# Performance work log

Measured on AMD Instinct MI355X. Metric: run time of the kernel, lower is better.

The kernel has to match this reference:

```python
import jax, jax.numpy as jnp
import numpy as np

NUM_HEADS = 16

def setup_inputs() -> dict:
    key = jax.random.key(0)
    k1, k2, k3 = jax.random.split(key, 3)
    B, N, C = 4, 1024, 1024
    x = jax.random.normal(k1, (B, N, C), dtype=jnp.float32)
    w_qkv = jax.random.normal(k2, (C, 3 * C), dtype=jnp.float32) * (C ** -0.5)
    b_qkv = jnp.zeros((3 * C,), dtype=jnp.float32)
    w_proj = jax.random.normal(k3, (C, C), dtype=jnp.float32) * (C ** -0.5)
    b_proj = jnp.zeros((C,), dtype=jnp.float32)
    return {"x": x, "w_qkv": w_qkv, "b_qkv": b_qkv, "w_proj": w_proj, "b_proj": b_proj}

def reference(x, w_qkv, b_qkv, w_proj, b_proj):
    B, N, C = x.shape
    H = NUM_HEADS
    D = C // H
    scale = D ** -0.5
    # qkv projection: [B,N,3C] -> [3,B,H,N,D]
    qkv = (x @ w_qkv + b_qkv).reshape(B, N, 3, H, D).transpose(2, 0, 3, 1, 4)
    q, k, v = qkv[0], qkv[1], qkv[2]
    q = q * scale
    attn = jnp.einsum('bhnd,bhmd->bhnm', q, k)  # full N x N scores
    attn = jax.nn.softmax(attn, axis=-1)
    out = jnp.einsum('bhnm,bhmd->bhnd', attn, v)  # [B,H,N,D]
    out = out.transpose(0, 2, 1, 3).reshape(B, N, C)
    return out @ w_proj + b_proj
```

## Files before the change

### kernel.cpp

```cpp
#include <hip/hip_runtime.h>

typedef unsigned short u16;
typedef unsigned int u32;
typedef __attribute__((ext_vector_type(8))) short bf16x8;
typedef __attribute__((ext_vector_type(4))) float f32x4;
typedef __attribute__((ext_vector_type(16))) float f32x16;

#define LOG2E 1.4426950408889634f
#define QSCALE (0.125f * LOG2E)

__device__ __forceinline__ u16 f2bf(float f) {
  union { float f; u32 u; } x; x.f = f;
  u32 r = x.u + 0x7fffu + ((x.u >> 16) & 1u);
  return (u16)(r >> 16);
}

__device__ __forceinline__ u32 cvtpk(float a, float b) {
  u32 r;
  asm("v_cvt_pk_bf16_f32 %0, %1, %2" : "=v"(r) : "v"(a), "v"(b));
  return r;
}

__device__ __forceinline__ bf16x8 mkfrag(u32 a, u32 b, u32 c, u32 d) {
  union { u32 w[4]; bf16x8 v; } u;
  u.w[0] = a; u.w[1] = b; u.w[2] = c; u.w[3] = d;
  return u.v;
}

__device__ __forceinline__ void gload_lds16(const void* g, void* l) {
  __builtin_amdgcn_global_load_lds((const __attribute__((address_space(1))) u32*)g,
                                   (__attribute__((address_space(3))) u32*)l, 16, 0, 0);
}

__device__ __forceinline__ void packP(const f32x16& s, int hi, bf16x8& P0, bf16x8& P1) {
  u32 w0 = cvtpk(s[0], s[1]),  w1 = cvtpk(s[2], s[3]);
  u32 w2 = cvtpk(s[4], s[5]),  w3 = cvtpk(s[6], s[7]);
  u32 w4 = cvtpk(s[8], s[9]),  w5 = cvtpk(s[10], s[11]);
  u32 w6 = cvtpk(s[12], s[13]), w7 = cvtpk(s[14], s[15]);
  u32 x0 = __shfl_xor((int)w0, 32), x1 = __shfl_xor((int)w1, 32);
  u32 x2 = __shfl_xor((int)w2, 32), x3 = __shfl_xor((int)w3, 32);
  u32 x4 = __shfl_xor((int)w4, 32), x5 = __shfl_xor((int)w5, 32);
  u32 x6 = __shfl_xor((int)w6, 32), x7 = __shfl_xor((int)w7, 32);
  P0 = mkfrag(hi ? x2 : w0, hi ? x3 : w1, hi ? w2 : x0, hi ? w3 : x1);
  P1 = mkfrag(hi ? x6 : w4, hi ? x7 : w5, hi ? w6 : x4, hi ? w7 : x5);
}

__global__ __launch_bounds__(256) void k_cvt_x(const float* __restrict__ in, u16* __restrict__ out) {
  int i = blockIdx.x * 256 + threadIdx.x;
  const float4* p = (const float4*)in;
  float4 a = p[i * 2], b = p[i * 2 + 1];
  uint4 o;
  o.x = (u32)f2bf(a.x) | ((u32)f2bf(a.y) << 16);
  o.y = (u32)f2bf(a.z) | ((u32)f2bf(a.w) << 16);
  o.z = (u32)f2bf(b.x) | ((u32)f2bf(b.y) << 16);
  o.w = (u32)f2bf(b.z) | ((u32)f2bf(b.w) << 16);
  ((uint4*)out)[i] = o;
}

__global__ __launch_bounds__(256) void k_transpose_cvt(const float* __restrict__ src, u16* __restrict__ dst,
                                                       int R, int Cc) {
  __shared__ float tile[32][33];
  int c0 = blockIdx.x * 32, r0 = blockIdx.y * 32;
  int tx = threadIdx.x, ty = threadIdx.y;
  #pragma unroll
  for (int j = 0; j < 4; ++j)
    tile[ty * 4 + j][tx] = src[(r0 + ty * 4 + j) * Cc + c0 + tx];
  __syncthreads();
  #pragma unroll
  for (int j = 0; j < 4; ++j) {
    int cl = ty * 4 + j;
    dst[(c0 + cl) * R + r0 + tx] = f2bf(tile[tx][cl]);
  }
}

template <int EPI, int NBN>
__global__ __launch_bounds__(512) void k_gemm(const u16* __restrict__ A, const u16* __restrict__ Bt,
                                              const float* __restrict__ bias,
                                              u16* __restrict__ oq, u16* __restrict__ ok,
                                              u16* __restrict__ ovt, float* __restrict__ of) {
  __shared__ u16 lds[24576];
  const int tid = threadIdx.x;
  const int l = tid & 63, w = tid >> 6;
  const int wm = w >> 2, wn = w & 3;
  const int lr = l & 15, lh = l >> 4;
  const int cpx = gridDim.x >> 3;
  const int wg = (blockIdx.x & 7) * cpx + (blockIdx.x >> 3);
  const int bn = wg % NBN, bm = wg / NBN;

  f32x4 acc[4][2] = {};
  const int e = tid * 8;
  const int srow = e >> 5;
  const int sgr  = (e >> 3) & 3;
  const int scol = (sgr ^ ((srow >> 1) & 3)) * 8;
  const u16* gA = A + (bm * 128 + srow) * 1024 + scol;
  const u16* gB = Bt + (bn * 128 + srow) * 1024 + scol;

  #define GSTAGE(kk, b)                                              \
    do {                                                             \
      gload_lds16(gA + (kk), lds + (b) * 8192 + e);                  \
      gload_lds16(gB + (kk), lds + (b) * 8192 + 4096 + e);           \
    } while (0)

  GSTAGE(0, 0);
  GSTAGE(32, 1);
  int cur = 0, nxt = 2;

  for (int it = 0; it < 32; ++it) {
    if (it < 31) asm volatile("s_waitcnt vmcnt(2)" ::: "memory");
    else         asm volatile("s_waitcnt vmcnt(0)" ::: "memory");
    __builtin_amdgcn_s_barrier();
    __builtin_amdgcn_sched_barrier(0);

    if (it < 30) GSTAGE((it + 2) * 32, nxt);

    const u16* Asc = lds + cur * 8192;
    bf16x8 af[4], bfr[2];
    #pragma unroll
    for (int mi = 0; mi < 4; ++mi) {
      int r = wm * 64 + mi * 16 + lr;
      af[mi] = *(const bf16x8*)(Asc + r * 32 + ((lh ^ ((r >> 1) & 3)) * 8));
    }
    #pragma unroll
    for (int ni = 0; ni < 2; ++ni) {
      int r = wn * 32 + ni * 16 + lr;
      bfr[ni] = *(const bf16x8*)(Asc + 4096 + r * 32 + ((lh ^ ((r >> 1) & 3)) * 8));
    }
    #pragma unroll
    for (int mi = 0; mi < 4; ++mi)
      #pragma unroll
      for (int ni = 0; ni < 2; ++ni)
        acc[mi][ni] = __builtin_amdgcn_mfma_f32_16x16x32_bf16(af[mi], bfr[ni], acc[mi][ni], 0, 0, 0);

    cur = (cur == 2) ? 0 : cur + 1;
    nxt = (nxt == 2) ? 0 : nxt + 1;
  }
  #undef GSTAGE

  if (EPI == 0) {
    #pragma unroll
    for (int ni = 0; ni < 2; ++ni) {
      int col = bn * 128 + wn * 32 + ni * 16 + lr;
      float bb = bias[col];
      #pragma unroll
      for (int mi = 0; mi < 4; ++mi) {
        int row = bm * 128 + wm * 64 + mi * 16 + lh * 4;
        #pragma unroll
        for (int r = 0; r < 4; ++r)
          of[(row + r) * (NBN * 128) + col] = acc[mi][ni][r] + bb;
      }
    }
  } else {
    const int s = bn >> 3;
    __syncthreads();
    if (s < 2) {
      u16* dst = (s == 0) ? oq : ok;
      const float sc = (s == 0) ? QSCALE : 1.0f;
      #pragma unroll
      for (int ni = 0; ni < 2; ++ni) {
        int cl = wn * 32 + ni * 16 + lr;
        float bb = bias[bn * 128 + cl];
        #pragma unroll
        for (int mi = 0; mi < 4; ++mi) {
          int rl = wm * 64 + mi * 16 + lh * 4;
          #pragma unroll
          for (int r = 0; r < 4; ++r)
            lds[(rl + r) * 136 + cl] = f2bf((acc[mi][ni][r] + bb) * sc);
        }
      }
      __syncthreads();
      const int row = tid >> 2, q4 = tid & 3;
      const int h0 = ((bn * 128) & 1023) >> 6;
      const int b = (bm * 128) >> 10, n0 = (bm * 128) & 1023;
      const u16* srow2 = lds + row * 136 + q4 * 32;
      u16* drow = dst + ((u32)((b * 16 + h0 + (q4 >> 1)) * 1024) + n0 + row) * 64 + (q4 & 1) * 32;
      #pragma unroll
      for (int j = 0; j < 4; ++j)
        *(uint4*)(drow + j * 8) = *(const uint4*)(srow2 + j * 8);
    } else {
      #pragma unroll
      for (int ni = 0; ni < 2; ++ni) {
        int cl = wn * 32 + ni * 16 + lr;
        float bb = bias[bn * 128 + cl];
        #pragma unroll
        for (int mi = 0; mi < 4; ++mi) {
          int rl = wm * 64 + mi * 16 + lh * 4;
          u32 p0 = (u32)f2bf(acc[mi][ni][0] + bb) | ((u32)f2bf(acc[mi][ni][1] + bb) << 16);
          u32 p1 = (u32)f2bf(acc[mi][ni][2] + bb) | ((u32)f2bf(acc[mi][ni][3] + bb) << 16);
          uint2 pk; pk.x = p0; pk.y = p1;
          *(uint2*)(lds + cl * 136 + rl) = pk;
        }
      }
      __syncthreads();
      const int cl = tid >> 2, q4 = tid & 3;
      const int c = bn * 128 + cl, cc = c & 1023, h = cc >> 6, d = cc & 63;
      const int b = (bm * 128) >> 10, n0 = (bm * 128) & 1023;
      const u16* srow2 = lds + cl * 136 + q4 * 32;
      u16* drow = ovt + ((b * 16 + h) * 64 + d) * 1024 + n0 + q4 * 32;
      #pragma unroll
      for (int j = 0; j < 4; ++j)
        *(uint4*)(drow + j * 8) = *(const uint4*)(srow2 + j * 8);
    }
  }
}

__global__ __launch_bounds__(256) void k_attn(const u16* __restrict__ q, const u16* __restrict__ k,
                                              const u16* __restrict__ vt, u16* __restrict__ ao) {
  __shared__ u16 Ks[2][4096], Vs[3][4096];
  const int tid = threadIdx.x, l = tid & 63, w = tid >> 6;
  const int lq = l & 31;
  const int hi = l >> 5;
  const int i = blockIdx.x;
  const int bh = (i & 7) * 8 + ((i >> 3) & 7);
  const int qb = i >> 6;

  const int qrow = qb * 128 + w * 32 + lq;
  const u16* qg = q + bh * 65536 + qrow * 64;
  bf16x8 qf[4];
  #pragma unroll
  for (int ks = 0; ks < 4; ++ks)
    qf[ks] = *(const bf16x8*)(qg + ks * 16 + hi * 8);

  float lsum = 0.f;
  f32x16 o0 = {}, o1 = {};
  bf16x8 pa[4];

  const u16* kg = k + bh * 65536;
  const u16* vg = vt + bh * 65536;

  const int ch0 = tid, ch1 = 256 + tid;
  const int r0_ = ch0 >> 3, s0_ = (ch0 & 7) ^ (r0_ & 7);
  const int r1_ = ch1 >> 3, s1_ = (ch1 & 7) ^ (r1_ & 7);

  #define STAGE(t, kb, vb)                                                     \
    do {                                                                       \
      gload_lds16(kg + (t) * 4096 + r0_ * 64 + s0_ * 8, Ks[kb] + ch0 * 8);     \
      gload_lds16(kg + (t) * 4096 + r1_ * 64 + s1_ * 8, Ks[kb] + ch1 * 8);     \
      gload_lds16(vg + r0_ * 1024 + (t) * 64 + s0_ * 8, Vs[vb] + ch0 * 8);     \
      gload_lds16(vg + r1_ * 1024 + (t) * 64 + s1_ * 8, Vs[vb] + ch1 * 8);     \
    } while (0)

  const int swz = (lq & 7) << 4;

  #define QKM(kb, SA, SB)                                                      \
    do {                                                                       \
      const char* Kb = (const char*)Ks[kb];                                    \
      _Pragma("unroll")                                                        \
      for (int ks2 = 0; ks2 < 4; ++ks2) {                                      \
        bf16x8 kf0 = *(const bf16x8*)(Kb + (((lq) * 128 + ks2 * 32 + hi * 16) ^ swz));      \
        bf16x8 kf1 = *(const bf16x8*)(Kb + (((32 + lq) * 128 + ks2 * 32 + hi * 16) ^ swz)); \
        SA = __builtin_amdgcn_mfma_f32_32x32x16_bf16(kf0, qf[ks2], SA, 0, 0, 0); \
        SB = __builtin_amdgcn_mfma_f32_32x32x16_bf16(kf1, qf[ks2], SB, 0, 0, 0); \
      }                                                                        \
    } while (0)

  #define SM(SA, SB)                                                           \
    do {                                                                       \
      float l0 = 0.f, l1 = 0.f, l2 = 0.f, l3 = 0.f;                            \
      _Pragma("unroll") for (int r = 0; r < 16; r += 4) {                      \
        float e0 = __builtin_amdgcn_exp2f(SA[r]);                              \
        float e1 = __builtin_amdgcn_exp2f(SA[r + 1]);                          \
        float e2 = __builtin_amdgcn_exp2f(SA[r + 2]);                          \
        float e3 = __builtin_amdgcn_exp2f(SA[r + 3]);                          \
        SA[r] = e0; SA[r + 1] = e1; SA[r + 2] = e2; SA[r + 3] = e3;            \
        l0 += e0; l1 += e1; l2 += e2; l3 += e3;                                \
      }                                                                        \
      _Pragma("unroll") for (int r = 0; r < 16; r += 4) {                      \
        float e0 = __builtin_amdgcn_exp2f(SB[r]);                              \
        float e1 = __builtin_amdgcn_exp2f(SB[r + 1]);                          \
        float e2 = __builtin_amdgcn_exp2f(SB[r + 2]);                          \
        float e3 = __builtin_amdgcn_exp2f(SB[r + 3]);                          \
        SB[r] = e0; SB[r + 1] = e1; SB[r + 2] = e2; SB[r + 3] = e3;            \
        l0 += e0; l1 += e1; l2 += e2; l3 += e3;                                \
      }                                                                        \
      lsum += (l0 + l1) + (l2 + l3);                                           \
      packP(SA, hi, pa[0], pa[1]);                                             \
      packP(SB, hi, pa[2], pa[3]);                                             \
    } while (0)

  #define PVM(vb)                                                              \
    do {                                                                       \
      const char* Vb = (const char*)Vs[vb];                                    \
      _Pragma("unroll")                                                        \
      for (int ks2 = 0; ks2 < 4; ++ks2) {                                      \
        bf16x8 vf0 = *(const bf16x8*)(Vb + (((lq) * 128 + ks2 * 32 + hi * 16) ^ swz));      \
        bf16x8 vf1 = *(const bf16x8*)(Vb + (((32 + lq) * 128 + ks2 * 32 + hi * 16) ^ swz)); \
        o0 = __builtin_amdgcn_mfma_f32_32x32x16_bf16(pa[ks2], vf0, o0, 0, 0, 0); \
        o1 = __builtin_amdgcn_mfma_f32_32x32x16_bf16(pa[ks2], vf1, o1, 0, 0, 0); \
      }                                                                        \
    } while (0)

  STAGE(0, 0, 0);
  STAGE(1, 1, 1);

  asm volatile("s_waitcnt vmcnt(6)" ::: "memory");
  __builtin_amdgcn_s_barrier();
  __builtin_amdgcn_sched_barrier(0);
  {
    f32x16 sA = {}, sB = {};
    QKM(0, sA, sB);
    SM(sA, sB);
  }

  for (int t = 0; t < 15; ++t) {
    const int vb = t % 3;
    const int kb1 = (t + 1) & 1;
    if (t < 14) asm volatile("s_waitcnt vmcnt(2)" ::: "memory");
    else        asm volatile("s_waitcnt vmcnt(0)" ::: "memory");
    __builtin_amdgcn_s_barrier();
    __builtin_amdgcn_sched_barrier(0);
    if (t < 14) STAGE(t + 2, (t + 2) & 1, (t + 2) % 3);

    f32x16 sA = {}, sB = {};
    __builtin_amdgcn_s_setprio(1);
    PVM(vb);
    QKM(kb1, sA, sB);
    __builtin_amdgcn_s_setprio(0);
    SM(sA, sB);
  }
  PVM(0);
  #undef STAGE
  #undef QKM
  #undef SM
  #undef PVM

  lsum += __shfl_xor(lsum, 32);
  const int b = bh >> 4, h = bh & 15;
  u16* aob = ao + (u32)(b * 1024 + qb * 128 + w * 32) * 1024 + h * 64;
  #pragma unroll
  for (int r = 0; r < 16; ++r) {
    int row = (r & 3) + 8 * (r >> 2) + 4 * hi;
    float inv = 1.0f / __shfl(lsum, row, 64);
    aob[row * 1024 + lq]      = f2bf(o0[r] * inv);
    aob[row * 1024 + 32 + lq] = f2bf(o1[r] * inv);
  }
}

extern "C" void kernel_launch(void* const* d_in, const int* in_sizes, int n_in,
                              void* d_out, int out_size, void* d_ws, size_t ws_size,
                              hipStream_t stream) {
  const float* x      = (const float*)d_in[0];
  const float* w_qkv  = (const float*)d_in[1];
  const float* b_qkv  = (const float*)d_in[2];
  const float* w_proj = (const float*)d_in[3];
  const float* b_proj = (const float*)d_in[4];
  float* out = (float*)d_out;
  char* ws = (char*)d_ws;

  u16* X16   = (u16*)ws;
  u16* Wqkv  = (u16*)(ws + 8388608);
  u16* Wproj = (u16*)(ws + 14680064);
  u16* Q     = (u16*)(ws + 16777216);
  u16* K     = (u16*)(ws + 25165824);
  u16* VT    = (u16*)(ws + 33554432);
  u16* AO    = X16;

  k_cvt_x<<<dim3(2048), dim3(256), 0, stream>>>(x, X16);
  k_transpose_cvt<<<dim3(96, 32), dim3(32, 8), 0, stream>>>(w_qkv, Wqkv, 1024, 3072);
  k_transpose_cvt<<<dim3(32, 32), dim3(32, 8), 0, stream>>>(w_proj, Wproj, 1024, 1024);
  k_gemm<1, 24><<<dim3(768), dim3(512), 0, stream>>>(X16, Wqkv, b_qkv, Q, K, VT, (float*)0);
  k_attn<<<dim3(512), dim3(256), 0, stream>>>(Q, K, VT, AO);
  k_gemm<0, 8><<<dim3(256), dim3(512), 0, stream>>>(AO, Wproj, b_proj, (u16*)0, (u16*)0, (u16*)0, out);
}
```

Baseline: 97.47 us.

## Split attention KV sequence across two wave groups and merge partial outputs

Attention blocks grow from 256 to 512 threads. Each group of four waves processes half of the 16 key/value tiles for the same 128 query rows, using separate LDS staging buffers. The second group then writes its partial outputs and row sums to LDS, and the first group adds them in and writes the normalized result. The aim is more waves per query tile and a shorter serial KV loop to hide latency, at the cost of more LDS, an extra reduction step, and fewer blocks per CU.

Result: slower. 99.50 us (+2.1%).

```diff
diff --git a/kernel.cpp b/kernel.cpp
--- a/kernel.cpp
+++ b/kernel.cpp
@@ -203,17 +203,18 @@
   }
 }
 
-__global__ __launch_bounds__(256) void k_attn(const u16* __restrict__ q, const u16* __restrict__ k,
+__global__ __launch_bounds__(512) void k_attn(const u16* __restrict__ q, const u16* __restrict__ k,
                                               const u16* __restrict__ vt, u16* __restrict__ ao) {
-  __shared__ u16 Ks[2][4096], Vs[3][4096];
+  __shared__ u16 lds[40960];
   const int tid = threadIdx.x, l = tid & 63, w = tid >> 6;
-  const int lq = l & 31;
-  const int hi = l >> 5;
+  const int lq = l & 31, hi = l >> 5;
+  const int g = w >> 2, wl = w & 3;
   const int i = blockIdx.x;
   const int bh = (i & 7) * 8 + ((i >> 3) & 7);
   const int qb = i >> 6;
-
-  const int qrow = qb * 128 + w * 32 + lq;
+  const int t0 = g * 8;
+
+  const int qrow = qb * 128 + wl * 32 + lq;
   const u16* qg = q + bh * 65536 + qrow * 64;
   bf16x8 qf[4];
   #pragma unroll
@@ -227,23 +228,27 @@
   const u16* kg = k + bh * 65536;
   const u16* vg = vt + bh * 65536;
 
-  const int ch0 = tid, ch1 = 256 + tid;
+  u16* Kl = lds + g * 8192;
+  u16* Vl = lds + 16384 + g * 12288;
+
+  const int tg = tid & 255;
+  const int ch0 = tg, ch1 = 256 + tg;
   const int r0_ = ch0 >> 3, s0_ = (ch0 & 7) ^ (r0_ & 7);
   const int r1_ = ch1 >> 3, s1_ = (ch1 & 7) ^ (r1_ & 7);
 
-  #define STAGE(t, kb, vb)                                                     \
-    do {                                                                       \
-      gload_lds16(kg + (t) * 4096 + r0_ * 64 + s0_ * 8, Ks[kb] + ch0 * 8);     \
-      gload_lds16(kg + (t) * 4096 + r1_ * 64 + s1_ * 8, Ks[kb] + ch1 * 8);     \
-      gload_lds16(vg + r0_ * 1024 + (t) * 64 + s0_ * 8, Vs[vb] + ch0 * 8);     \
-      gload_lds16(vg + r1_ * 1024 + (t) * 64 + s1_ * 8, Vs[vb] + ch1 * 8);     \
+  #define STAGE(t, kb, vb)                                                         \
+    do {                                                                           \
+      gload_lds16(kg + (t) * 4096 + r0_ * 64 + s0_ * 8, Kl + (kb) * 4096 + ch0 * 8); \
+      gload_lds16(kg + (t) * 4096 + r1_ * 64 + s1_ * 8, Kl + (kb) * 4096 + ch1 * 8); \
+      gload_lds16(vg + r0_ * 1024 + (t) * 64 + s0_ * 8, Vl + (vb) * 4096 + ch0 * 8); \
+      gload_lds16(vg + r1_ * 1024 + (t) * 64 + s1_ * 8, Vl + (vb) * 4096 + ch1 * 8); \
     } while (0)
 
   const int swz = (lq & 7) << 4;
 
   #define QKM(kb, SA, SB)                                                      \
     do {                                                                       \
-      const char* Kb = (const char*)Ks[kb];                                    \
+      const char* Kb = (const char*)(Kl + (kb) * 4096);                        \
       _Pragma("unroll")                                                        \
       for (int ks2 = 0; ks2 < 4; ++ks2) {                                      \
         bf16x8 kf0 = *(const bf16x8*)(Kb + (((lq) * 128 + ks2 * 32 + hi * 16) ^ swz));      \
@@ -279,7 +284,7 @@
 
   #define PVM(vb)                                                              \
     do {                                                                       \
-      const char* Vb = (const char*)Vs[vb];                                    \
+      const char* Vb = (const char*)(Vl + (vb) * 4096);                        \
       _Pragma("unroll")                                                        \
       for (int ks2 = 0; ks2 < 4; ++ks2) {                                      \
         bf16x8 vf0 = *(const bf16x8*)(Vb + (((lq) * 128 + ks2 * 32 + hi * 16) ^ swz));      \
@@ -289,8 +294,8 @@
       }                                                                        \
     } while (0)
 
-  STAGE(0, 0, 0);
-  STAGE(1, 1, 1);
+  STAGE(t0, 0, 0);
+  STAGE(t0 + 1, 1, 1);
 
   asm volatile("s_waitcnt vmcnt(6)" ::: "memory");
   __builtin_amdgcn_s_barrier();
@@ -301,14 +306,14 @@
     SM(sA, sB);
   }
 
-  for (int t = 0; t < 15; ++t) {
-    const int vb = t % 3;
-    const int kb1 = (t + 1) & 1;
-    if (t < 14) asm volatile("s_waitcnt vmcnt(2)" ::: "memory");
+  for (int tl = 0; tl < 7; ++tl) {
+    const int vb = tl % 3;
+    const int kb1 = (tl + 1) & 1;
+    if (tl < 6) asm volatile("s_waitcnt vmcnt(2)" ::: "memory");
     else        asm volatile("s_waitcnt vmcnt(0)" ::: "memory");
     __builtin_amdgcn_s_barrier();
     __builtin_amdgcn_sched_barrier(0);
-    if (t < 14) STAGE(t + 2, (t + 2) & 1, (t + 2) % 3);
+    if (tl < 6) STAGE(t0 + tl + 2, (tl + 2) & 1, (tl + 2) % 3);
 
     f32x16 sA = {}, sB = {};
     __builtin_amdgcn_s_setprio(1);
@@ -317,21 +322,37 @@
     __builtin_amdgcn_s_setprio(0);
     SM(sA, sB);
   }
-  PVM(0);
+  PVM(1);
   #undef STAGE
   #undef QKM
   #undef SM
   #undef PVM
 
   lsum += __shfl_xor(lsum, 32);
-  const int b = bh >> 4, h = bh & 15;
-  u16* aob = ao + (u32)(b * 1024 + qb * 128 + w * 32) * 1024 + h * 64;
-  #pragma unroll
-  for (int r = 0; r < 16; ++r) {
-    int row = (r & 3) + 8 * (r >> 2) + 4 * hi;
-    float inv = 1.0f / __shfl(lsum, row, 64);
-    aob[row * 1024 + lq]      = f2bf(o0[r] * inv);
-    aob[row * 1024 + 32 + lq] = f2bf(o1[r] * inv);
+
+  __syncthreads();
+  float* mf = (float*)lds;
+  const int mbase = (wl * 64 + l) * 33;
+  if (g == 1) {
+    #pragma unroll
+    for (int r = 0; r < 16; ++r) { mf[mbase + r] = o0[r]; mf[mbase + 16 + r] = o1[r]; }
+    mf[8448 + wl * 64 + l] = lsum;
+  }
+  __syncthreads();
+  if (g == 0) {
+    #pragma unroll
+    for (int r = 0; r < 16; ++r) { o0[r] += mf[mbase + r]; o1[r] += mf[mbase + 16 + r]; }
+    lsum += mf[8448 + wl * 64 + l];
+
+    const int b = bh >> 4, h = bh & 15;
+    u16* aob = ao + (u32)(b * 1024 + qb * 128 + wl * 32) * 1024 + h * 64;
+    #pragma unroll
+    for (int r = 0; r < 16; ++r) {
+      int row = (r & 3) + 8 * (r >> 2) + 4 * hi;
+      float inv = 1.0f / __shfl(lsum, row, 64);
+      aob[row * 1024 + lq]      = f2bf(o0[r] * inv);
+      aob[row * 1024 + 32 + lq] = f2bf(o1[r] * inv);
+    }
   }
 }
 
@@ -358,6 +379,6 @@
   k_transpose_cvt<<<dim3(96, 32), dim3(32, 8), 0, stream>>>(w_qkv, Wqkv, 1024, 3072);
   k_transpose_cvt<<<dim3(32, 32), dim3(32, 8), 0, stream>>>(w_proj, Wproj, 1024, 1024);
   k_gemm<1, 24><<<dim3(768), dim3(512), 0, stream>>>(X16, Wqkv, b_qkv, Q, K, VT, (float*)0);
-  k_attn<<<dim3(512), dim3(256), 0, stream>>>(Q, K, VT, AO);
+  k_attn<<<dim3(512), dim3(512), 0, stream>>>(Q, K, VT, AO);
   k_gemm<0, 8><<<dim3(256), dim3(512), 0, stream>>>(AO, Wproj, b_proj, (u16*)0, (u16*)0, (u16*)0, out);
 }
```

## Load K/V fragments directly from global into registers, dropping LDS staging

Applied to the files above, without the earlier changes.

The attention kernel no longer stages K and V tiles through shared memory with async global-to-LDS copies and barriers. Each lane now loads its MFMA operand fragments for K and V^T straight from global memory into registers, double-buffering K across iterations. This removes the LDS traffic and block-wide synchronization. In exchange, each of the four waves reads the same K/V data from global/L2 redundantly, the loads are less coalesced, and register pressure rises.

Result: slower. 129.6 us (+33.0%).

```diff
diff --git a/kernel.cpp b/kernel.cpp
--- a/kernel.cpp
+++ b/kernel.cpp
@@ -205,10 +205,8 @@
 
 __global__ __launch_bounds__(256) void k_attn(const u16* __restrict__ q, const u16* __restrict__ k,
                                               const u16* __restrict__ vt, u16* __restrict__ ao) {
-  __shared__ u16 Ks[2][4096], Vs[3][4096];
   const int tid = threadIdx.x, l = tid & 63, w = tid >> 6;
-  const int lq = l & 31;
-  const int hi = l >> 5;
+  const int lq = l & 31, hi = l >> 5;
   const int i = blockIdx.x;
   const int bh = (i & 7) * 8 + ((i >> 3) & 7);
   const int qb = i >> 6;
@@ -224,101 +222,93 @@
   f32x16 o0 = {}, o1 = {};
   bf16x8 pa[4];
 
-  const u16* kg = k + bh * 65536;
-  const u16* vg = vt + bh * 65536;
-
-  const int ch0 = tid, ch1 = 256 + tid;
-  const int r0_ = ch0 >> 3, s0_ = (ch0 & 7) ^ (r0_ & 7);
-  const int r1_ = ch1 >> 3, s1_ = (ch1 & 7) ^ (r1_ & 7);
-
-  #define STAGE(t, kb, vb)                                                     \
-    do {                                                                       \
-      gload_lds16(kg + (t) * 4096 + r0_ * 64 + s0_ * 8, Ks[kb] + ch0 * 8);     \
-      gload_lds16(kg + (t) * 4096 + r1_ * 64 + s1_ * 8, Ks[kb] + ch1 * 8);     \
-      gload_lds16(vg + r0_ * 1024 + (t) * 64 + s0_ * 8, Vs[vb] + ch0 * 8);     \
-      gload_lds16(vg + r1_ * 1024 + (t) * 64 + s1_ * 8, Vs[vb] + ch1 * 8);     \
-    } while (0)
-
-  const int swz = (lq & 7) << 4;
-
-  #define QKM(kb, SA, SB)                                                      \
-    do {                                                                       \
-      const char* Kb = (const char*)Ks[kb];                                    \
-      _Pragma("unroll")                                                        \
-      for (int ks2 = 0; ks2 < 4; ++ks2) {                                      \
-        bf16x8 kf0 = *(const bf16x8*)(Kb + (((lq) * 128 + ks2 * 32 + hi * 16) ^ swz));      \
-        bf16x8 kf1 = *(const bf16x8*)(Kb + (((32 + lq) * 128 + ks2 * 32 + hi * 16) ^ swz)); \
-        SA = __builtin_amdgcn_mfma_f32_32x32x16_bf16(kf0, qf[ks2], SA, 0, 0, 0); \
-        SB = __builtin_amdgcn_mfma_f32_32x32x16_bf16(kf1, qf[ks2], SB, 0, 0, 0); \
-      }                                                                        \
-    } while (0)
-
-  #define SM(SA, SB)                                                           \
-    do {                                                                       \
-      float l0 = 0.f, l1 = 0.f, l2 = 0.f, l3 = 0.f;                            \
-      _Pragma("unroll") for (int r = 0; r < 16; r += 4) {                      \
-        float e0 = __builtin_amdgcn_exp2f(SA[r]);                              \
-        float e1 = __builtin_amdgcn_exp2f(SA[r + 1]);                          \
-        float e2 = __builtin_amdgcn_exp2f(SA[r + 2]);                          \
-        float e3 = __builtin_amdgcn_exp2f(SA[r + 3]);                          \
-        SA[r] = e0; SA[r + 1] = e1; SA[r + 2] = e2; SA[r + 3] = e3;            \
-        l0 += e0; l1 += e1; l2 += e2; l3 += e3;                                \
-      }                                                                        \
-      _Pragma("unroll") for (int r = 0; r < 16; r += 4) {                      \
-        float e0 = __builtin_amdgcn_exp2f(SB[r]);                              \
-        float e1 = __builtin_amdgcn_exp2f(SB[r + 1]);                          \
-        float e2 = __builtin_amdgcn_exp2f(SB[r + 2]);                          \
-        float e3 = __builtin_amdgcn_exp2f(SB[r + 3]);                          \
-        SB[r] = e0; SB[r + 1] = e1; SB[r + 2] = e2; SB[r + 3] = e3;            \
-        l0 += e0; l1 += e1; l2 += e2; l3 += e3;                                \
-      }                                                                        \
-      lsum += (l0 + l1) + (l2 + l3);                                           \
-      packP(SA, hi, pa[0], pa[1]);                                             \
-      packP(SB, hi, pa[2], pa[3]);                                             \
-    } while (0)
-
-  #define PVM(vb)                                                              \
-    do {                                                                       \
-      const char* Vb = (const char*)Vs[vb];                                    \
-      _Pragma("unroll")                                                        \
-      for (int ks2 = 0; ks2 < 4; ++ks2) {                                      \
-        bf16x8 vf0 = *(const bf16x8*)(Vb + (((lq) * 128 + ks2 * 32 + hi * 16) ^ swz));      \
-        bf16x8 vf1 = *(const bf16x8*)(Vb + (((32 + lq) * 128 + ks2 * 32 + hi * 16) ^ swz)); \
-        o0 = __builtin_amdgcn_mfma_f32_32x32x16_bf16(pa[ks2], vf0, o0, 0, 0, 0); \
-        o1 = __builtin_amdgcn_mfma_f32_32x32x16_bf16(pa[ks2], vf1, o1, 0, 0, 0); \
-      }                                                                        \
-    } while (0)
-
-  STAGE(0, 0, 0);
-  STAGE(1, 1, 1);
-
-  asm volatile("s_waitcnt vmcnt(6)" ::: "memory");
-  __builtin_amdgcn_s_barrier();
-  __builtin_amdgcn_sched_barrier(0);
-  {
-    f32x16 sA = {}, sB = {};
-    QKM(0, sA, sB);
-    SM(sA, sB);
-  }
-
-  for (int t = 0; t < 15; ++t) {
-    const int vb = t % 3;
-    const int kb1 = (t + 1) & 1;
-    if (t < 14) asm volatile("s_waitcnt vmcnt(2)" ::: "memory");
-    else        asm volatile("s_waitcnt vmcnt(0)" ::: "memory");
-    __builtin_amdgcn_s_barrier();
-    __builtin_amdgcn_sched_barrier(0);
-    if (t < 14) STAGE(t + 2, (t + 2) & 1, (t + 2) % 3);
-
-    f32x16 sA = {}, sB = {};
-    __builtin_amdgcn_s_setprio(1);
-    PVM(vb);
-    QKM(kb1, sA, sB);
-    __builtin_amdgcn_s_setprio(0);
-    SM(sA, sB);
-  }
-  PVM(0);
-  #undef STAGE
+  const u16* kbase = k + bh * 65536 + lq * 64 + hi * 8;
+  const u16* vbase = vt + bh * 65536 + lq * 1024 + hi * 8;
+
+  bf16x8 kA[8], kB[8], vC[8];
+
+  #define LOADK(dst, t) do {                                              \
+    const u16* p_ = kbase + (t) * 4096;                                   \
+    dst[0] = *(const bf16x8*)(p_);        dst[1] = *(const bf16x8*)(p_ + 16);        \
+    dst[2] = *(const bf16x8*)(p_ + 32);   dst[3] = *(const bf16x8*)(p_ + 48);        \
+    dst[4] = *(const bf16x8*)(p_ + 2048); dst[5] = *(const bf16x8*)(p_ + 2048 + 16); \
+    dst[6] = *(const bf16x8*)(p_ + 2048 + 32); dst[7] = *(const bf16x8*)(p_ + 2048 + 48); \
+  } while (0)
+
+  #define LOADV(dst, t) do {                                              \
+    const u16* p_ = vbase + (t) * 64;                                     \
+    dst[0] = *(const bf16x8*)(p_);         dst[1] = *(const bf16x8*)(p_ + 16);         \
+    dst[2] = *(const bf16x8*)(p_ + 32);    dst[3] = *(const bf16x8*)(p_ + 48);         \
+    dst[4] = *(const bf16x8*)(p_ + 32768); dst[5] = *(const bf16x8*)(p_ + 32768 + 16); \
+    dst[6] = *(const bf16x8*)(p_ + 32768 + 32); dst[7] = *(const bf16x8*)(p_ + 32768 + 48); \
+  } while (0)
+
+  #define QKM(kbuf, SA, SB) do {                                          \
+    __builtin_amdgcn_s_setprio(1);                                        \
+    _Pragma("unroll")                                                     \
+    for (int j = 0; j < 4; ++j) {                                         \
+      SA = __builtin_amdgcn_mfma_f32_32x32x16_bf16(kbuf[j],     qf[j], SA, 0, 0, 0); \
+      SB = __builtin_amdgcn_mfma_f32_32x32x16_bf16(kbuf[4 + j], qf[j], SB, 0, 0, 0); \
+    }                                                                     \
+    __builtin_amdgcn_s_setprio(0);                                        \
+  } while (0)
+
+  #define SM(SA, SB) do {                                                 \
+    float l0 = 0.f, l1 = 0.f, l2 = 0.f, l3 = 0.f;                         \
+    _Pragma("unroll") for (int r = 0; r < 16; r += 4) {                   \
+      float e0 = __builtin_amdgcn_exp2f(SA[r]);                           \
+      float e1 = __builtin_amdgcn_exp2f(SA[r + 1]);                       \
+      float e2 = __builtin_amdgcn_exp2f(SA[r + 2]);                       \
+      float e3 = __builtin_amdgcn_exp2f(SA[r + 3]);                       \
+      SA[r] = e0; SA[r + 1] = e1; SA[r + 2] = e2; SA[r + 3] = e3;         \
+      l0 += e0; l1 += e1; l2 += e2; l3 += e3;                             \
+    }                                                                     \
+    _Pragma("unroll") for (int r = 0; r < 16; r += 4) {                   \
+      float e0 = __builtin_amdgcn_exp2f(SB[r]);                           \
+      float e1 = __builtin_amdgcn_exp2f(SB[r + 1]);                       \
+      float e2 = __builtin_amdgcn_exp2f(SB[r + 2]);                       \
+      float e3 = __builtin_amdgcn_exp2f(SB[r + 3]);                       \
+      SB[r] = e0; SB[r + 1] = e1; SB[r + 2] = e2; SB[r + 3] = e3;         \
+      l0 += e0; l1 += e1; l2 += e2; l3 += e3;                             \
+    }                                                                     \
+    lsum += (l0 + l1) + (l2 + l3);                                        \
+    packP(SA, hi, pa[0], pa[1]);                                          \
+    packP(SB, hi, pa[2], pa[3]);                                          \
+  } while (0)
+
+  #define PVM(vbuf) do {                                                  \
+    __builtin_amdgcn_s_setprio(1);                                        \
+    _Pragma("unroll")                                                     \
+    for (int j = 0; j < 4; ++j) {                                         \
+      o0 = __builtin_amdgcn_mfma_f32_32x32x16_bf16(pa[j], vbuf[j],     o0, 0, 0, 0); \
+      o1 = __builtin_amdgcn_mfma_f32_32x32x16_bf16(pa[j], vbuf[4 + j], o1, 0, 0, 0); \
+    }                                                                     \
+    __builtin_amdgcn_s_setprio(0);                                        \
+  } while (0)
+
+  LOADK(kA, 0);
+
+  #pragma unroll 1
+  for (int t = 0; t < 16; t += 2) {
+    LOADV(vC, t);
+    LOADK(kB, t + 1);
+    {
+      f32x16 sA = {}, sB = {};
+      QKM(kA, sA, sB);
+      SM(sA, sB);
+      PVM(vC);
+    }
+    LOADV(vC, t + 1);
+    if (t + 2 < 16) LOADK(kA, t + 2);
+    {
+      f32x16 sA = {}, sB = {};
+      QKM(kB, sA, sB);
+      SM(sA, sB);
+      PVM(vC);
+    }
+  }
+  #undef LOADK
+  #undef LOADV
   #undef QKM
   #undef SM
   #undef PVM
```

## Split attention over two KV halves and merge partial outputs

Applied to the files above, without the earlier changes.

Adds a split-KV attention kernel that launches 1024 blocks, each covering half of the key/value sequence, and writes unnormalized fp32 partial outputs and row sums to workspace. A merge kernel then adds the two halves, normalizes, and writes the bf16 attention output. This raises the block count from 512 to fill more compute units, at the cost of extra fp32 traffic (about 32MB written and then read back) and one more launch. The split path is only taken when the workspace is large enough; otherwise the original kernel runs. It skips the max-subtraction, which is safe because the original kernel did not subtract a max either.

Measured after the change: 107.9 us. +10.7%, slower.

```diff
diff --git a/kernel.cpp b/kernel.cpp
--- a/kernel.cpp
+++ b/kernel.cpp
@@ -203,35 +203,11 @@
   }
 }
 
-__global__ __launch_bounds__(256) void k_attn(const u16* __restrict__ q, const u16* __restrict__ k,
-                                              const u16* __restrict__ vt, u16* __restrict__ ao) {
-  __shared__ u16 Ks[2][4096], Vs[3][4096];
-  const int tid = threadIdx.x, l = tid & 63, w = tid >> 6;
-  const int lq = l & 31;
-  const int hi = l >> 5;
-  const int i = blockIdx.x;
-  const int bh = (i & 7) * 8 + ((i >> 3) & 7);
-  const int qb = i >> 6;
-
-  const int qrow = qb * 128 + w * 32 + lq;
-  const u16* qg = q + bh * 65536 + qrow * 64;
-  bf16x8 qf[4];
-  #pragma unroll
-  for (int ks = 0; ks < 4; ++ks)
-    qf[ks] = *(const bf16x8*)(qg + ks * 16 + hi * 8);
-
-  float lsum = 0.f;
-  f32x16 o0 = {}, o1 = {};
-  bf16x8 pa[4];
-
-  const u16* kg = k + bh * 65536;
-  const u16* vg = vt + bh * 65536;
-
-  const int ch0 = tid, ch1 = 256 + tid;
-  const int r0_ = ch0 >> 3, s0_ = (ch0 & 7) ^ (r0_ & 7);
-  const int r1_ = ch1 >> 3, s1_ = (ch1 & 7) ^ (r1_ & 7);
-
-  #define STAGE(t, kb, vb)                                                     \
+#define ATTN_MACROS                                                            \
+  const int swz = (lq & 7) << 4;                                               \
+  (void)swz;
+
+#define STAGE_DEF(t, kb, vb)                                                   \
     do {                                                                       \
       gload_lds16(kg + (t) * 4096 + r0_ * 64 + s0_ * 8, Ks[kb] + ch0 * 8);     \
       gload_lds16(kg + (t) * 4096 + r1_ * 64 + s1_ * 8, Ks[kb] + ch1 * 8);     \
@@ -239,9 +215,7 @@
       gload_lds16(vg + r1_ * 1024 + (t) * 64 + s1_ * 8, Vs[vb] + ch1 * 8);     \
     } while (0)
 
-  const int swz = (lq & 7) << 4;
-
-  #define QKM(kb, SA, SB)                                                      \
+#define QKM_DEF(kb, SA, SB)                                                    \
     do {                                                                       \
       const char* Kb = (const char*)Ks[kb];                                    \
       _Pragma("unroll")                                                        \
@@ -253,7 +227,7 @@
       }                                                                        \
     } while (0)
 
-  #define SM(SA, SB)                                                           \
+#define SM_DEF(SA, SB)                                                         \
     do {                                                                       \
       float l0 = 0.f, l1 = 0.f, l2 = 0.f, l3 = 0.f;                            \
       _Pragma("unroll") for (int r = 0; r < 16; r += 4) {                      \
@@ -277,7 +251,7 @@
       packP(SB, hi, pa[2], pa[3]);                                             \
     } while (0)
 
-  #define PVM(vb)                                                              \
+#define PVM_DEF(vb)                                                            \
     do {                                                                       \
       const char* Vb = (const char*)Vs[vb];                                    \
       _Pragma("unroll")                                                        \
@@ -289,16 +263,45 @@
       }                                                                        \
     } while (0)
 
-  STAGE(0, 0, 0);
-  STAGE(1, 1, 1);
+__global__ __launch_bounds__(256) void k_attn(const u16* __restrict__ q, const u16* __restrict__ k,
+                                              const u16* __restrict__ vt, u16* __restrict__ ao) {
+  __shared__ u16 Ks[2][4096], Vs[3][4096];
+  const int tid = threadIdx.x, l = tid & 63, w = tid >> 6;
+  const int lq = l & 31, hi = l >> 5;
+  const int i = blockIdx.x;
+  const int bh = (i & 7) * 8 + ((i >> 3) & 7);
+  const int qb = i >> 6;
+
+  const int qrow = qb * 128 + w * 32 + lq;
+  const u16* qg = q + bh * 65536 + qrow * 64;
+  bf16x8 qf[4];
+  #pragma unroll
+  for (int ks = 0; ks < 4; ++ks)
+    qf[ks] = *(const bf16x8*)(qg + ks * 16 + hi * 8);
+
+  float lsum = 0.f;
+  f32x16 o0 = {}, o1 = {};
+  bf16x8 pa[4];
+
+  const u16* kg = k + bh * 65536;
+  const u16* vg = vt + bh * 65536;
+
+  const int ch0 = tid, ch1 = 256 + tid;
+  const int r0_ = ch0 >> 3, s0_ = (ch0 & 7) ^ (r0_ & 7);
+  const int r1_ = ch1 >> 3, s1_ = (ch1 & 7) ^ (r1_ & 7);
+
+  const int swz = (lq & 7) << 4;
+
+  STAGE_DEF(0, 0, 0);
+  STAGE_DEF(1, 1, 1);
 
   asm volatile("s_waitcnt vmcnt(6)" ::: "memory");
   __builtin_amdgcn_s_barrier();
   __builtin_amdgcn_sched_barrier(0);
   {
     f32x16 sA = {}, sB = {};
-    QKM(0, sA, sB);
-    SM(sA, sB);
+    QKM_DEF(0, sA, sB);
+    SM_DEF(sA, sB);
   }
 
   for (int t = 0; t < 15; ++t) {
@@ -308,20 +311,16 @@
     else        asm volatile("s_waitcnt vmcnt(0)" ::: "memory");
     __builtin_amdgcn_s_barrier();
     __builtin_amdgcn_sched_barrier(0);
-    if (t < 14) STAGE(t + 2, (t + 2) & 1, (t + 2) % 3);
+    if (t < 14) STAGE_DEF(t + 2, (t + 2) & 1, (t + 2) % 3);
 
     f32x16 sA = {}, sB = {};
     __builtin_amdgcn_s_setprio(1);
-    PVM(vb);
-    QKM(kb1, sA, sB);
+    PVM_DEF(vb);
+    QKM_DEF(kb1, sA, sB);
     __builtin_amdgcn_s_setprio(0);
-    SM(sA, sB);
-  }
-  PVM(0);
-  #undef STAGE
-  #undef QKM
-  #undef SM
-  #undef PVM
+    SM_DEF(sA, sB);
+  }
+  PVM_DEF(0);
 
   lsum += __shfl_xor(lsum, 32);
   const int b = bh >> 4, h = bh & 15;
@@ -333,6 +332,99 @@
     aob[row * 1024 + lq]      = f2bf(o0[r] * inv);
     aob[row * 1024 + 32 + lq] = f2bf(o1[r] * inv);
   }
+}
+
+__global__ __launch_bounds__(256) void k_attn_split(const u16* __restrict__ q, const u16* __restrict__ k,
+                                                    const u16* __restrict__ vt,
+                                                    float* __restrict__ PO, float* __restrict__ LS) {
+  __shared__ u16 Ks[2][4096], Vs[3][4096];
+  const int tid = threadIdx.x, l = tid & 63, w = tid >> 6;
+  const int lq = l & 31, hi = l >> 5;
+  const int hf = blockIdx.x >> 9;
+  const int i = blockIdx.x & 511;
+  const int bh = (i & 7) * 8 + ((i >> 3) & 7);
+  const int qb = i >> 6;
+  const int t0 = hf * 8;
+
+  const int qrow = qb * 128 + w * 32 + lq;
+  const u16* qg = q + bh * 65536 + qrow * 64;
+  bf16x8 qf[4];
+  #pragma unroll
+  for (int ks = 0; ks < 4; ++ks)
+    qf[ks] = *(const bf16x8*)(qg + ks * 16 + hi * 8);
+
+  float lsum = 0.f;
+  f32x16 o0 = {}, o1 = {};
+  bf16x8 pa[4];
+
+  const u16* kg = k + bh * 65536;
+  const u16* vg = vt + bh * 65536;
+
+  const int ch0 = tid, ch1 = 256 + tid;
+  const int r0_ = ch0 >> 3, s0_ = (ch0 & 7) ^ (r0_ & 7);
+  const int r1_ = ch1 >> 3, s1_ = (ch1 & 7) ^ (r1_ & 7);
+
+  const int swz = (lq & 7) << 4;
+
+  STAGE_DEF(t0, 0, 0);
+  STAGE_DEF(t0 + 1, 1, 1);
+
+  asm volatile("s_waitcnt vmcnt(6)" ::: "memory");
+  __builtin_amdgcn_s_barrier();
+  __builtin_amdgcn_sched_barrier(0);
+  {
+    f32x16 sA = {}, sB = {};
+    QKM_DEF(0, sA, sB);
+    SM_DEF(sA, sB);
+  }
+
+  for (int tl = 0; tl < 7; ++tl) {
+    const int vb = tl % 3;
+    const int kb1 = (tl + 1) & 1;
+    if (tl < 6) asm volatile("s_waitcnt vmcnt(2)" ::: "memory");
+    else        asm volatile("s_waitcnt vmcnt(0)" ::: "memory");
+    __builtin_amdgcn_s_barrier();
+    __builtin_amdgcn_sched_barrier(0);
+    if (tl < 6) STAGE_DEF(t0 + tl + 2, (tl + 2) & 1, (tl + 2) % 3);
+
+    f32x16 sA = {}, sB = {};
+    __builtin_amdgcn_s_setprio(1);
+    PVM_DEF(vb);
+    QKM_DEF(kb1, sA, sB);
+    __builtin_amdgcn_s_setprio(0);
+    SM_DEF(sA, sB);
+  }
+  PVM_DEF(1);
+
+  lsum += __shfl_xor(lsum, 32);
+  float* PO_ = PO + (u32)((hf * 64 + bh) * 1024 + qb * 128 + w * 32) * 64;
+  #pragma unroll
+  for (int r = 0; r < 16; ++r) {
+    int row = (r & 3) + 8 * (r >> 2) + 4 * hi;
+    PO_[row * 64 + lq]      = o0[r];
+    PO_[row * 64 + 32 + lq] = o1[r];
+  }
+  if (hi == 0)
+    LS[(hf * 64 + bh) * 1024 + qb * 128 + w * 32 + lq] = lsum;
+}
+
+__global__ __launch_bounds__(256) void k_merge(const float* __restrict__ PO, const float* __restrict__ LS,
+                                               u16* __restrict__ ao) {
+  int idx = blockIdx.x * 256 + threadIdx.x;
+  int dg = idx & 7, row = (idx >> 3) & 1023, bh = idx >> 13;
+  const float* p0 = PO + ((u32)(bh * 1024 + row) * 64) + dg * 8;
+  const float* p1 = p0 + 4194304;
+  float l = LS[bh * 1024 + row] + LS[65536 + bh * 1024 + row];
+  float inv = 1.0f / l;
+  float4 a0 = *(const float4*)p0, a1 = *(const float4*)(p0 + 4);
+  float4 b0 = *(const float4*)p1, b1 = *(const float4*)(p1 + 4);
+  uint4 o;
+  o.x = (u32)f2bf((a0.x + b0.x) * inv) | ((u32)f2bf((a0.y + b0.y) * inv) << 16);
+  o.y = (u32)f2bf((a0.z + b0.z) * inv) | ((u32)f2bf((a0.w + b0.w) * inv) << 16);
+  o.z = (u32)f2bf((a1.x + b1.x) * inv) | ((u32)f2bf((a1.y + b1.y) * inv) << 16);
+  o.w = (u32)f2bf((a1.z + b1.z) * inv) | ((u32)f2bf((a1.w + b1.w) * inv) << 16);
+  int b = bh >> 4, h = bh & 15;
+  *(uint4*)(ao + (u32)(b * 1024 + row) * 1024 + h * 64 + dg * 8) = o;
 }
 
 extern "C" void kernel_launch(void* const* d_in, const int* in_sizes, int n_in,
@@ -352,12 +444,19 @@
   u16* Q     = (u16*)(ws + 16777216);
   u16* K     = (u16*)(ws + 25165824);
   u16* VT    = (u16*)(ws + 33554432);
+  float* PO  = (float*)(ws + 41943040);
+  float* LS  = (float*)(ws + 75497472);
   u16* AO    = X16;
 
   k_cvt_x<<<dim3(2048), dim3(256), 0, stream>>>(x, X16);
   k_transpose_cvt<<<dim3(96, 32), dim3(32, 8), 0, stream>>>(w_qkv, Wqkv, 1024, 3072);
   k_transpose_cvt<<<dim3(32, 32), dim3(32, 8), 0, stream>>>(w_proj, Wproj, 1024, 1024);
   k_gemm<1, 24><<<dim3(768), dim3(512), 0, stream>>>(X16, Wqkv, b_qkv, Q, K, VT, (float*)0);
-  k_attn<<<dim3(512), dim3(256), 0, stream>>>(Q, K, VT, AO);
+  if (ws_size >= 76021760) {
+    k_attn_split<<<dim3(1024), dim3(256), 0, stream>>>(Q, K, VT, PO, LS);
+    k_merge<<<dim3(2048), dim3(256), 0, stream>>>(PO, LS, AO);
+  } else {
+    k_attn<<<dim3(512), dim3(256), 0, stream>>>(Q, K, VT, AO);
+  }
   k_gemm<0, 8><<<dim3(256), dim3(512), 0, stream>>>(AO, Wproj, b_proj, (u16*)0, (u16*)0, (u16*)0, out);
 }
```
